# Kernel tuning notes

Hardware: AMD Instinct MI355X
Metric: run time of the kernel (lower is better)

Reference implementation:

```python
import jax, jax.numpy as jnp
import numpy as np

H = 256
EPS = 1e-5
RBF_GAMMA = 10.0
RBF_CENTERS = jnp.asarray(np.arange(0.0, np.pi, 0.1), dtype=jnp.float32)  # 32 centers


def layer_norm(x, g, b):
    m = x.mean(-1, keepdims=True)
    v = ((x - m) ** 2).mean(-1, keepdims=True)
    return (x - m) * jax.lax.rsqrt(v + EPS) * g + b


def gin(src, dst, n_nodes, node_feat, edge_feat, w1, b1, w2, b2):
    # message = h_src + h_edge ; sum-aggregate at dst ; 2-layer MLP
    msg = node_feat[src] + edge_feat                                  # [E, H]
    agg = jax.ops.segment_sum(msg, dst, num_segments=n_nodes)        # [N, H]
    return jax.nn.relu(agg @ w1 + b1) @ w2 + b2


def graph_normal(gid, n_graphs, x):
    # divide each node feature by sqrt(#nodes in its graph)
    cnt = jax.ops.segment_sum(jnp.ones((x.shape[0],), x.dtype), gid, num_segments=n_graphs)
    return x * jax.lax.rsqrt(jnp.maximum(cnt, 1.0))[gid][:, None]


def geognn_block(src, dst, gid, n_graphs, node_hidden, edge_feat, w1, b1, w2, b2, ln_g, ln_b):
    out = gin(src, dst, node_hidden.shape[0], node_hidden, edge_feat, w1, b1, w2, b2)
    out = layer_norm(out, ln_g, ln_b)
    out = graph_normal(gid, n_graphs, out)
    # activation=False, dropout is identity in eval mode
    return out + node_hidden


def setup_inputs() -> dict:
    key = jax.random.key(0)
    ks = jax.random.split(key, 24)
    N, E, A, G = 65536, 131072, 262144, 2048
    nC = RBF_CENTERS.shape[0]
    s = 1.0 / np.sqrt(H)
    inp = {
        "node_hidden": jax.random.normal(ks[0], (N, H), jnp.float32),
        "edge_hidden": jax.random.normal(ks[1], (E, H), jnp.float32),
        "bond_angle": jax.random.uniform(ks[2], (A,), jnp.float32) * np.float32(np.pi),
        "ab_src": jax.random.randint(ks[3], (N * 2,), 0, N).astype(jnp.int64)[:E],
        "ab_dst": jax.random.randint(ks[4], (E,), 0, N).astype(jnp.int64),
        "ba_src": jax.random.randint(ks[5], (A,), 0, E).astype(jnp.int64),
        "ba_dst": jax.random.randint(ks[6], (A,), 0, E).astype(jnp.int64),
        "node_gid": jnp.sort(jax.random.randint(ks[7], (N,), 0, G)).astype(jnp.int64),
        "bond_gid": jnp.sort(jax.random.randint(ks[8], (E,), 0, G)).astype(jnp.int64),
        "num_graphs": G,
        # bond-angle RBF linear
        "rbf_w": jax.random.normal(ks[9], (nC, H), jnp.float32) / np.sqrt(nC),
        "rbf_b": jnp.zeros((H,), jnp.float32),
        # bond_angle_gnn (GIN MLP + LayerNorm)
        "ba_w1": jax.random.normal(ks[10], (H, 2 * H), jnp.float32) * s,
        "ba_b1": jnp.zeros((2 * H,), jnp.float32),
        "ba_w2": jax.random.normal(ks[11], (2 * H, H), jnp.float32) * s,
        "ba_b2": jnp.zeros((H,), jnp.float32),
        "ba_ln_g": jnp.ones((H,), jnp.float32),
        "ba_ln_b": jnp.zeros((H,), jnp.float32),
        # atom_bond_gnn
        "ab_w1": jax.random.normal(ks[12], (H, 2 * H), jnp.float32) * s,
        "ab_b1": jnp.zeros((2 * H,), jnp.float32),
        "ab_w2": jax.random.normal(ks[13], (2 * H, H), jnp.float32) * s,
        "ab_b2": jnp.zeros((H,), jnp.float32),
        "ab_ln_g": jnp.ones((H,), jnp.float32),
        "ab_ln_b": jnp.zeros((H,), jnp.float32),
    }
    return inp


def reference(node_hidden, edge_hidden, bond_angle, ab_src, ab_dst, ba_src, ba_dst,
              node_gid, bond_gid, num_graphs, rbf_w, rbf_b,
              ba_w1, ba_b1, ba_w2, ba_b2, ba_ln_g, ba_ln_b,
              ab_w1, ab_b1, ab_w2, ab_b2, ab_ln_g, ab_ln_b):
    # RBF encode bond angles -> angle edge features [A, H]
    rbf = jnp.exp(-RBF_GAMMA * (bond_angle[:, None] - RBF_CENTERS[None, :]) ** 2)
    angle_hidden = rbf @ rbf_w + rbf_b
    # bond-angle GNN updates bond features (nodes of bond_angle graph)
    edge_out = geognn_block(ba_src, ba_dst, bond_gid, num_graphs,
                            edge_hidden, angle_hidden,
                            ba_w1, ba_b1, ba_w2, ba_b2, ba_ln_g, ba_ln_b)
    # atom-bond GNN updates atom features using updated bond features as edge feats
    node_out = geognn_block(ab_src, ab_dst, node_gid, num_graphs,
                            node_hidden, edge_out,
                            ab_w1, ab_b1, ab_w2, ab_b2, ab_ln_g, ab_ln_b)
    # average pooling over atoms per graph
    cnt = jax.ops.segment_sum(jnp.ones((node_out.shape[0],), node_out.dtype), node_gid,
                              num_segments=num_graphs)
    graph_repr = jax.ops.segment_sum(node_out, node_gid, num_segments=num_graphs) / jnp.maximum(cnt, 1.0)[:, None]
    return node_out, edge_out, graph_repr
```

## Files before the change

### kernel.cpp

```cpp
#include <hip/hip_runtime.h>

#define HDIM 256
#define LNEPS 1e-5f

typedef float f32x4 __attribute__((ext_vector_type(4)));
typedef short bf16x8 __attribute__((ext_vector_type(8)));

static __device__ __forceinline__ unsigned short f2b(float f) {
  union { float f; unsigned u; } v; v.f = f;
  return (unsigned short)((v.u + 0x7fffu + ((v.u >> 16) & 1u)) >> 16);
}
static __device__ __forceinline__ unsigned pk2(float lo, float hi) {
  return (unsigned)f2b(lo) | ((unsigned)f2b(hi) << 16);
}

__global__ void pack1_kernel(const float* __restrict__ in, unsigned short* __restrict__ out) {
  int o = blockIdx.x * 256 + threadIdx.x;
  int ke = o & 7, n1l = (o >> 3) & 127, lg = (o >> 10) & 3, sl = o >> 12;
  int h = sl >> 3, kk = sl & 7;
  int k = kk * 32 + lg * 8 + ke, n1 = h * 128 + n1l;
  out[o] = f2b(in[k * 512 + n1]);
}

__global__ void pack2_kernel(const float* __restrict__ in, unsigned short* __restrict__ out) {
  int o = blockIdx.x * 256 + threadIdx.x;
  int ke = o & 7, n2l = (o >> 3) & 127, lg = (o >> 10) & 3, sl = o >> 12;
  int h = sl >> 3, r = sl & 7, h2 = r >> 2, kk2 = r & 3;
  int k2 = h * 128 + kk2 * 32 + lg * 8 + ke, n2 = h2 * 128 + n2l;
  out[o] = f2b(in[k2 * 256 + n2]);
}

__global__ void count_kernel(const int* __restrict__ node_gid, const int* __restrict__ bond_gid,
                             int* cnt_node, int* cnt_bond, int N, int E) {
  int i = blockIdx.x * 256 + threadIdx.x;
  if (i < N) atomicAdd(&cnt_node[node_gid[i]], 1);
  if (i < E) atomicAdd(&cnt_bond[bond_gid[i]], 1);
}

__global__ void factor_kernel(const int* __restrict__ cnt_node, const int* __restrict__ cnt_bond,
                              float* fac_node, float* fac_bond, float* recip_node, int G) {
  int g = blockIdx.x * 256 + threadIdx.x;
  if (g >= G) return;
  float cn = fmaxf((float)cnt_node[g], 1.f);
  float cb = fmaxf((float)cnt_bond[g], 1.f);
  fac_node[g] = rsqrtf(cn);
  fac_bond[g] = rsqrtf(cb);
  recip_node[g] = 1.f / cn;
}

__global__ void deg_kernel(const int* __restrict__ dst, int* __restrict__ deg, int n) {
  int i = blockIdx.x * 256 + threadIdx.x;
  if (i < n) atomicAdd(&deg[dst[i]], 1);
}

__global__ void scan1_kernel(const int* __restrict__ deg, int* __restrict__ excl,
                             int* __restrict__ bsum, int n) {
  int t = threadIdx.x;
  int i = blockIdx.x * 256 + t;
  int v = (i < n) ? deg[i] : 0;
  int lane = t & 63, w = t >> 6;
  int s = v;
#pragma unroll
  for (int d = 1; d < 64; d <<= 1) {
    int u = __shfl_up(s, d);
    if (lane >= d) s += u;
  }
  __shared__ int wsum[4];
  if (lane == 63) wsum[w] = s;
  __syncthreads();
  int base = 0;
  for (int ww = 0; ww < w; ++ww) base += wsum[ww];
  if (i < n) excl[i] = base + s - v;
  if (t == 255) bsum[blockIdx.x] = base + s;
}

__global__ void scan2_kernel(int* __restrict__ bsum, int nb) {
  int t = threadIdx.x;
  int v = (t < nb) ? bsum[t] : 0;
  int lane = t & 63, w = t >> 6;
  int s = v;
#pragma unroll
  for (int d = 1; d < 64; d <<= 1) {
    int u = __shfl_up(s, d);
    if (lane >= d) s += u;
  }
  __shared__ int wsum[16];
  if (lane == 63) wsum[w] = s;
  __syncthreads();
  int base = 0;
  for (int ww = 0; ww < w; ++ww) base += wsum[ww];
  if (t < nb) bsum[t] = base + s - v;
}

__global__ void scan3_kernel(int* __restrict__ excl, const int* __restrict__ bsum, int n) {
  int i = blockIdx.x * 256 + threadIdx.x;
  if (i < n) excl[i] += bsum[blockIdx.x];
}

__global__ void fill_kernel(const int* __restrict__ dst, const int* __restrict__ off,
                            int* __restrict__ cursor, int* __restrict__ csr, int n) {
  int i = blockIdx.x * 256 + threadIdx.x;
  if (i >= n) return;
  int d = dst[i];
  int p = atomicAdd(&cursor[d], 1);
  csr[off[d] + p] = i;
}

__global__ __launch_bounds__(256) void angle_gather_kernel(
    const float* __restrict__ bond_angle, const int* __restrict__ ba_src,
    const float* __restrict__ edge_hidden,
    const int* __restrict__ off, const int* __restrict__ deg, const int* __restrict__ csr,
    const float* __restrict__ rbf_w, const float* __restrict__ rbf_b,
    float* __restrict__ agg_e, int E) {
  __shared__ float rbfw_s[32 * 256];
  int t = threadIdx.x;
  int w = t >> 6, lane = t & 63;
#pragma unroll
  for (int i = 0; i < 8; ++i)
    *(f32x4*)&rbfw_s[(t + i * 256) * 4] = *(const f32x4*)&rbf_w[(t + i * 256) * 4];
  __syncthreads();
  int c4 = lane * 4;
  f32x4 bv = *(const f32x4*)&rbf_b[c4];
  float cc = 0.1f * (float)(lane & 31);
  for (int rr = 0; rr < 2; ++rr) {
    int d = blockIdx.x * 8 + w * 2 + rr;
    if (d >= E) break;
    int start = off[d], cnt = deg[d];
    f32x4 acc = (f32x4)0.f;
    float rbfs = 0.f;
    for (int base = 0; base < cnt; base += 64) {
      int n = cnt - base; if (n > 64) n = 64;
      float av = 0.f;
      int s = 0;
      if (lane < n) {
        int a = csr[start + base + lane];
        av = bond_angle[a];
        s = ba_src[a];
      }
#pragma unroll 4
      for (int i = 0; i < n; ++i) {
        float avi = __shfl(av, i);
        int si = __shfl(s, i);
        if (lane < 32) {
          float dd = avi - cc;
          rbfs += __expf(-10.f * dd * dd);
        }
        acc += *(const f32x4*)&edge_hidden[(size_t)si * HDIM + c4];
      }
    }
#pragma unroll 8
    for (int k = 0; k < 32; ++k) {
      float rv = __shfl(rbfs, k);
      f32x4 wv = *(const f32x4*)&rbfw_s[k * 256 + c4];
      acc[0] += rv * wv[0]; acc[1] += rv * wv[1];
      acc[2] += rv * wv[2]; acc[3] += rv * wv[3];
    }
    float fc = (float)cnt;
    acc[0] += fc * bv[0]; acc[1] += fc * bv[1];
    acc[2] += fc * bv[2]; acc[3] += fc * bv[3];
    *(f32x4*)&agg_e[(size_t)d * HDIM + c4] = acc;
  }
}

__global__ __launch_bounds__(256) void node_gather_kernel(
    const float* __restrict__ node_hidden, const float* __restrict__ edge_out,
    const int* __restrict__ ab_src,
    const int* __restrict__ off, const int* __restrict__ deg, const int* __restrict__ csr,
    float* __restrict__ agg_n, int N) {
  int w = threadIdx.x >> 6, lane = threadIdx.x & 63;
  int d = blockIdx.x * 4 + w;
  if (d >= N) return;
  int c4 = lane * 4;
  int start = off[d], cnt = deg[d];
  f32x4 acc = (f32x4)0.f;
  for (int base = 0; base < cnt; base += 64) {
    int n = cnt - base; if (n > 64) n = 64;
    int e = 0, s = 0;
    if (lane < n) {
      e = csr[start + base + lane];
      s = ab_src[e];
    }
#pragma unroll 4
    for (int i = 0; i < n; ++i) {
      int ei = __shfl(e, i);
      int si = __shfl(s, i);
      f32x4 a = *(const f32x4*)&edge_out[(size_t)ei * HDIM + c4];
      f32x4 b = *(const f32x4*)&node_hidden[(size_t)si * HDIM + c4];
      acc += a;
      acc += b;
    }
  }
  *(f32x4*)&agg_n[(size_t)d * HDIM + c4] = acc;
}

template <int POOL>
__global__ __launch_bounds__(256, 4) void mlp_kernel(
    const float* agg_in, float* out_rows,
    const float* __restrict__ residual, const int* __restrict__ gid,
    const float* __restrict__ gfactor,
    const unsigned short* __restrict__ w1p, const float* __restrict__ b1,
    const unsigned short* __restrict__ w2p, const float* __restrict__ b2,
    const float* __restrict__ ln_g, const float* __restrict__ ln_b,
    float* pool_out, int M) {
  __shared__ __align__(16) char smem[40960];
  char* Xb = smem;
  char* Hb = smem + 16384;
  char* Wb = smem + 24576;
  float* Outs = (float*)smem;
  float* fstat = (float*)(smem + 40448);
  float* gfs = (float*)(smem + 40704);
  int* gid_s = (int*)(smem + 40832);

  int t = threadIdx.x;
  int row0 = blockIdx.x * 32;
  int w = t >> 6, lane = t & 63;
  int l15 = lane & 15, lg = lane >> 4;

  auto slab_ptr = [&](int ss) -> const uint4* {
    int hh = ss >> 4, r = ss & 15;
    const unsigned short* p = (r < 8) ? (w1p + (size_t)(hh * 8 + r) * 4096)
                                      : (w2p + (size_t)(hh * 8 + (r - 8)) * 4096);
    return (const uint4*)p;
  };

  uint4 rA0, rA1, rB0, rB1;

  {
    const uint4* g0 = slab_ptr(0);
    uint4 s0a = g0[t], s0b = g0[t + 256];
    const uint4* g1 = slab_ptr(1);
    rA0 = g1[t]; rA1 = g1[t + 256];
    int row = t >> 3;
    int c0 = (t & 7) * 32;
    int gr = row0 + row; if (gr >= M) gr = M - 1;
    const float* src = agg_in + (size_t)gr * HDIM + c0;
#pragma unroll
    for (int i = 0; i < 4; ++i) {
      f32x4 a = *(const f32x4*)(src + i * 8);
      f32x4 b = *(const f32x4*)(src + i * 8 + 4);
      int byte = (row * 512 + (c0 + i * 8) * 2) ^ ((row & 7) << 4);
      *(uint4*)(Xb + byte) =
          make_uint4(pk2(a[0], a[1]), pk2(a[2], a[3]), pk2(b[0], b[1]), pk2(b[2], b[3]));
    }
    *(uint4*)(Wb + t * 16) = s0a;
    *(uint4*)(Wb + (t + 256) * 16) = s0b;
  }
  __syncthreads();

  f32x4 acc2[2][4];
#pragma unroll
  for (int mt = 0; mt < 2; ++mt)
#pragma unroll
    for (int nf = 0; nf < 4; ++nf) acc2[mt][nf] = (f32x4)0.f;

  int s = 0;
  for (int h = 0; h < 4; ++h) {
    f32x4 acc1[2][2];
#pragma unroll
    for (int tt = 0; tt < 2; ++tt)
#pragma unroll
      for (int mt = 0; mt < 2; ++mt) acc1[tt][mt] = (f32x4)0.f;

    for (int kk = 0; kk < 8; ++kk) {
      if (s + 2 < 64) { const uint4* g = slab_ptr(s + 2); rB0 = g[t]; rB1 = g[t + 256]; }
      const char* buf = Wb + (s & 1) * 8192;
      bf16x8 xfr[2], afr[2];
#pragma unroll
      for (int mt = 0; mt < 2; ++mt) {
        int m = mt * 16 + l15;
        int byte = (m * 512 + kk * 64 + lg * 16) ^ ((m & 7) << 4);
        xfr[mt] = *(const bf16x8*)(Xb + byte);
      }
#pragma unroll
      for (int tt = 0; tt < 2; ++tt)
        afr[tt] = *(const bf16x8*)(buf + lg * 2048 + (w * 32 + tt * 16 + l15) * 16);
#pragma unroll
      for (int tt = 0; tt < 2; ++tt)
#pragma unroll
        for (int mt = 0; mt < 2; ++mt)
          acc1[tt][mt] = __builtin_amdgcn_mfma_f32_16x16x32_bf16(afr[tt], xfr[mt], acc1[tt][mt], 0, 0, 0);

      if (kk == 7) {
#pragma unroll
        for (int tt = 0; tt < 2; ++tt) {
          f32x4 b1v = *(const f32x4*)&b1[h * 128 + w * 32 + tt * 16 + lg * 4];
#pragma unroll
          for (int mt = 0; mt < 2; ++mt) {
            f32x4 v = acc1[tt][mt] + b1v;
            v[0] = fmaxf(v[0], 0.f); v[1] = fmaxf(v[1], 0.f);
            v[2] = fmaxf(v[2], 0.f); v[3] = fmaxf(v[3], 0.f);
            int m = mt * 16 + l15;
            int n1l = w * 32 + tt * 16 + lg * 4;
            int byte = (m * 256 + n1l * 2) ^ ((m & 7) << 4);
            *(uint2*)(Hb + byte) = make_uint2(pk2(v[0], v[1]), pk2(v[2], v[3]));
          }
        }
      }
      if (s + 1 < 64) {
        char* nb = Wb + ((s + 1) & 1) * 8192;
        *(uint4*)(nb + t * 16) = rA0;
        *(uint4*)(nb + (t + 256) * 16) = rA1;
      }
      __syncthreads();
      rA0 = rB0; rA1 = rB1;
      ++s;
    }

#pragma unroll
    for (int h2 = 0; h2 < 2; ++h2) {
#pragma unroll
      for (int kk2 = 0; kk2 < 4; ++kk2) {
        if (s + 2 < 64) { const uint4* g = slab_ptr(s + 2); rB0 = g[t]; rB1 = g[t + 256]; }
        const char* buf = Wb + (s & 1) * 8192;
        bf16x8 hfr[2], wfr[2];
#pragma unroll
        for (int mt = 0; mt < 2; ++mt) {
          int m = mt * 16 + l15;
          int byte = (m * 256 + kk2 * 64 + lg * 16) ^ ((m & 7) << 4);
          hfr[mt] = *(const bf16x8*)(Hb + byte);
        }
#pragma unroll
        for (int nf = 0; nf < 2; ++nf)
          wfr[nf] = *(const bf16x8*)(buf + lg * 2048 + (w * 32 + nf * 16 + l15) * 16);
#pragma unroll
        for (int mt = 0; mt < 2; ++mt)
#pragma unroll
          for (int nf = 0; nf < 2; ++nf)
            acc2[mt][h2 * 2 + nf] =
                __builtin_amdgcn_mfma_f32_16x16x32_bf16(hfr[mt], wfr[nf], acc2[mt][h2 * 2 + nf], 0, 0, 0);
        if (s + 1 < 64) {
          char* nb = Wb + ((s + 1) & 1) * 8192;
          *(uint4*)(nb + t * 16) = rA0;
          *(uint4*)(nb + (t + 256) * 16) = rA1;
        }
        __syncthreads();
        rA0 = rB0; rA1 = rB1;
        ++s;
      }
    }
  }

#pragma unroll
  for (int nf = 0; nf < 4; ++nf) {
    int col = (nf >> 1) * 128 + w * 32 + (nf & 1) * 16 + l15;
    float b2v = b2[col];
#pragma unroll
    for (int mt = 0; mt < 2; ++mt)
#pragma unroll
      for (int jr = 0; jr < 4; ++jr)
        Outs[(mt * 16 + lg * 4 + jr) * 256 + col] = acc2[mt][nf][jr] + b2v;
  }
  if (t < 32) {
    int r = row0 + t;
    int g = (r < M) ? gid[r] : 0;
    gid_s[t] = g;
    gfs[t] = gfactor[g];
  }
  __syncthreads();

  {
    int row = t >> 3, sub = t & 7;
    float ssum = 0.f, ss = 0.f;
#pragma unroll
    for (int i = 0; i < 8; ++i) {
      f32x4 v = *(const f32x4*)&Outs[row * 256 + sub * 32 + i * 4];
      ssum += v[0] + v[1] + v[2] + v[3];
      ss += v[0] * v[0] + v[1] * v[1] + v[2] * v[2] + v[3] * v[3];
    }
    ssum += __shfl_xor(ssum, 1); ss += __shfl_xor(ss, 1);
    ssum += __shfl_xor(ssum, 2); ss += __shfl_xor(ss, 2);
    ssum += __shfl_xor(ssum, 4); ss += __shfl_xor(ss, 4);
    if (sub == 0) {
      float mean = ssum * (1.f / 256.f);
      float var = ss * (1.f / 256.f) - mean * mean;
      fstat[row * 2] = mean;
      fstat[row * 2 + 1] = rsqrtf(var + LNEPS);
    }
  }
  __syncthreads();

  {
    float g_t = ln_g[t], bb_t = ln_b[t];
    float psum = 0.f;
    int curg = -1;
#pragma unroll 4
    for (int p = 0; p < 32; ++p) {
      int gr = row0 + p;
      if (gr < M) {
        float v = Outs[p * 256 + t];
        v = (v - fstat[p * 2]) * fstat[p * 2 + 1] * g_t + bb_t;
        v *= gfs[p];
        v += residual[(size_t)gr * HDIM + t];
        out_rows[(size_t)gr * HDIM + t] = v;
        if (POOL) {
          int g = gid_s[p];
          if (g != curg) {
            if (curg >= 0) atomicAdd(&pool_out[(size_t)curg * HDIM + t], psum);
            psum = 0.f;
            curg = g;
          }
          psum += v;
        }
      }
    }
    if (POOL && curg >= 0) atomicAdd(&pool_out[(size_t)curg * HDIM + t], psum);
  }
}

__global__ void pooldiv_kernel(float* out_graph, const float* __restrict__ recip_node) {
  int g = blockIdx.x, t = threadIdx.x;
  out_graph[(size_t)g * HDIM + t] *= recip_node[g];
}

extern "C" void kernel_launch(void* const* d_in, const int* in_sizes, int n_in,
                              void* d_out, int out_size, void* d_ws, size_t ws_size,
                              hipStream_t stream) {
  const float* node_hidden = (const float*)d_in[0];
  const float* edge_hidden = (const float*)d_in[1];
  const float* bond_angle = (const float*)d_in[2];
  const int* ab_src = (const int*)d_in[3];
  const int* ab_dst = (const int*)d_in[4];
  const int* ba_src = (const int*)d_in[5];
  const int* ba_dst = (const int*)d_in[6];
  const int* node_gid = (const int*)d_in[7];
  const int* bond_gid = (const int*)d_in[8];
  const float* rbf_w = (const float*)d_in[10];
  const float* rbf_b = (const float*)d_in[11];
  const float* ba_w1 = (const float*)d_in[12];
  const float* ba_b1 = (const float*)d_in[13];
  const float* ba_w2 = (const float*)d_in[14];
  const float* ba_b2 = (const float*)d_in[15];
  const float* ba_ln_g = (const float*)d_in[16];
  const float* ba_ln_b = (const float*)d_in[17];
  const float* ab_w1 = (const float*)d_in[18];
  const float* ab_b1 = (const float*)d_in[19];
  const float* ab_w2 = (const float*)d_in[20];
  const float* ab_b2 = (const float*)d_in[21];
  const float* ab_ln_g = (const float*)d_in[22];
  const float* ab_ln_b = (const float*)d_in[23];

  int N = in_sizes[0] / HDIM;
  int E = in_sizes[1] / HDIM;
  int A = in_sizes[2];
  int G = out_size / HDIM - N - E;

  float* out_node = (float*)d_out;
  float* out_edge = out_node + (size_t)N * HDIM;
  float* out_graph = out_edge + (size_t)E * HDIM;

  char* ws = (char*)d_ws;
  int* cnt_node = (int*)ws;
  int* cnt_bond = cnt_node + G;
  int* deg_e = cnt_bond + G;
  int* cur_e = deg_e + E;
  int* deg_n = cur_e + E;
  int* cur_n = deg_n + N;
  size_t zero_bytes = (size_t)(2 * G + 2 * E + 2 * N) * 4;
  float* fac_node = (float*)(cur_n + N);
  float* fac_bond = fac_node + G;
  float* recip_node = fac_bond + G;
  int* off_e = (int*)(recip_node + G);
  int* csr_e = off_e + E;
  int* off_n = csr_e + A;
  int* csr_n = off_n + N;
  int* bsum = csr_n + E;
  size_t off = ((size_t)((char*)(bsum + 1024) - ws) + 255) & ~(size_t)255;
  unsigned short* w1p_ba = (unsigned short*)(ws + off); off += (size_t)512 * 256 * 2;
  unsigned short* w2p_ba = (unsigned short*)(ws + off); off += (size_t)256 * 512 * 2;
  unsigned short* w1p_ab = (unsigned short*)(ws + off); off += (size_t)512 * 256 * 2;
  unsigned short* w2p_ab = (unsigned short*)(ws + off); off += (size_t)256 * 512 * 2;

  hipMemsetAsync(d_ws, 0, zero_bytes, stream);
  hipMemsetAsync(out_graph, 0, (size_t)G * HDIM * 4, stream);

  pack1_kernel<<<512, 256, 0, stream>>>(ba_w1, w1p_ba);
  pack2_kernel<<<512, 256, 0, stream>>>(ba_w2, w2p_ba);
  pack1_kernel<<<512, 256, 0, stream>>>(ab_w1, w1p_ab);
  pack2_kernel<<<512, 256, 0, stream>>>(ab_w2, w2p_ab);

  count_kernel<<<(E + 255) / 256, 256, 0, stream>>>(node_gid, bond_gid, cnt_node, cnt_bond, N, E);
  factor_kernel<<<(G + 255) / 256, 256, 0, stream>>>(cnt_node, cnt_bond, fac_node, fac_bond,
                                                     recip_node, G);

  deg_kernel<<<(A + 255) / 256, 256, 0, stream>>>(ba_dst, deg_e, A);
  int nbE = (E + 255) / 256;
  scan1_kernel<<<nbE, 256, 0, stream>>>(deg_e, off_e, bsum, E);
  scan2_kernel<<<1, 1024, 0, stream>>>(bsum, nbE);
  scan3_kernel<<<nbE, 256, 0, stream>>>(off_e, bsum, E);
  fill_kernel<<<(A + 255) / 256, 256, 0, stream>>>(ba_dst, off_e, cur_e, csr_e, A);

  angle_gather_kernel<<<(E + 7) / 8, 256, 0, stream>>>(bond_angle, ba_src, edge_hidden,
                                                       off_e, deg_e, csr_e, rbf_w, rbf_b,
                                                       out_edge, E);
  mlp_kernel<0><<<(E + 31) / 32, 256, 0, stream>>>(out_edge, out_edge, edge_hidden, bond_gid,
                                                   fac_bond, w1p_ba, ba_b1, w2p_ba, ba_b2,
                                                   ba_ln_g, ba_ln_b, nullptr, E);

  deg_kernel<<<(E + 255) / 256, 256, 0, stream>>>(ab_dst, deg_n, E);
  int nbN = (N + 255) / 256;
  scan1_kernel<<<nbN, 256, 0, stream>>>(deg_n, off_n, bsum, N);
  scan2_kernel<<<1, 1024, 0, stream>>>(bsum, nbN);
  scan3_kernel<<<nbN, 256, 0, stream>>>(off_n, bsum, N);
  fill_kernel<<<(E + 255) / 256, 256, 0, stream>>>(ab_dst, off_n, cur_n, csr_n, E);

  node_gather_kernel<<<(N + 3) / 4, 256, 0, stream>>>(node_hidden, out_edge, ab_src,
                                                      off_n, deg_n, csr_n, out_node, N);
  mlp_kernel<1><<<(N + 31) / 32, 256, 0, stream>>>(out_node, out_node, node_hidden, node_gid,
                                                   fac_node, w1p_ab, ab_b1, w2p_ab, ab_b2,
                                                   ab_ln_g, ab_ln_b, out_graph, N);

  pooldiv_kernel<<<G, 256, 0, stream>>>(out_graph, recip_node);
}
```

Measured before the change: 610.7 us.

## Load MLP weight fragments directly from global into registers, drop LDS weight staging

The weight packing is reordered so that each wave's lanes can read their MFMA B-fragments straight from global memory. The MLP kernel drops the LDS double-buffered weight slabs and the per-slab block barrier, and prefetches fragments two steps ahead in registers. LayerNorm statistics are now computed from the accumulators with shuffles and a small cross-wave partial-sum array instead of re-reading the staged output. This cuts LDS use and most __syncthreads, at the cost of every wave fetching its own weight fragments from cache and using more registers.

```diff
diff --git a/kernel.cpp b/kernel.cpp
--- a/kernel.cpp
+++ b/kernel.cpp
@@ -16,17 +16,21 @@
 
 __global__ void pack1_kernel(const float* __restrict__ in, unsigned short* __restrict__ out) {
   int o = blockIdx.x * 256 + threadIdx.x;
-  int ke = o & 7, n1l = (o >> 3) & 127, lg = (o >> 10) & 3, sl = o >> 12;
+  int ke = o & 7, lane = (o >> 3) & 63, ttw = (o >> 9) & 7, sl = o >> 12;
   int h = sl >> 3, kk = sl & 7;
-  int k = kk * 32 + lg * 8 + ke, n1 = h * 128 + n1l;
+  int l15 = lane & 15, lg = lane >> 4;
+  int n1 = h * 128 + (ttw >> 1) * 32 + (ttw & 1) * 16 + l15;
+  int k = kk * 32 + lg * 8 + ke;
   out[o] = f2b(in[k * 512 + n1]);
 }
 
 __global__ void pack2_kernel(const float* __restrict__ in, unsigned short* __restrict__ out) {
   int o = blockIdx.x * 256 + threadIdx.x;
-  int ke = o & 7, n2l = (o >> 3) & 127, lg = (o >> 10) & 3, sl = o >> 12;
-  int h = sl >> 3, r = sl & 7, h2 = r >> 2, kk2 = r & 3;
-  int k2 = h * 128 + kk2 * 32 + lg * 8 + ke, n2 = h2 * 128 + n2l;
+  int ke = o & 7, lane = (o >> 3) & 63, ttw = (o >> 9) & 7, sl = o >> 12;
+  int h = sl >> 3, h2 = (sl >> 2) & 1, kk2 = sl & 3;
+  int l15 = lane & 15, lg = lane >> 4;
+  int n2 = h2 * 128 + (ttw >> 1) * 32 + (ttw & 1) * 16 + l15;
+  int k2 = h * 128 + kk2 * 32 + lg * 8 + ke;
   out[o] = f2b(in[k2 * 256 + n2]);
 }
 
@@ -202,34 +206,31 @@
     const unsigned short* __restrict__ w2p, const float* __restrict__ b2,
     const float* __restrict__ ln_g, const float* __restrict__ ln_b,
     float* pool_out, int M) {
-  __shared__ __align__(16) char smem[40960];
+  __shared__ __align__(16) char smem[34304];
   char* Xb = smem;
   char* Hb = smem + 16384;
-  char* Wb = smem + 24576;
   float* Outs = (float*)smem;
-  float* fstat = (float*)(smem + 40448);
-  float* gfs = (float*)(smem + 40704);
-  int* gid_s = (int*)(smem + 40832);
+  float* psA = (float*)(smem + 32768);
+  float* psB = (float*)(smem + 33280);
+  float* fstat = (float*)(smem + 33792);
+  float* gfs = (float*)(smem + 34048);
+  int* gid_s = (int*)(smem + 34176);
 
   int t = threadIdx.x;
   int row0 = blockIdx.x * 32;
   int w = t >> 6, lane = t & 63;
   int l15 = lane & 15, lg = lane >> 4;
 
-  auto slab_ptr = [&](int ss) -> const uint4* {
-    int hh = ss >> 4, r = ss & 15;
-    const unsigned short* p = (r < 8) ? (w1p + (size_t)(hh * 8 + r) * 4096)
-                                      : (w2p + (size_t)(hh * 8 + (r - 8)) * 4096);
-    return (const uint4*)p;
-  };
-
-  uint4 rA0, rA1, rB0, rB1;
+#define W1F(hh, kk, tt) \
+  (*(const bf16x8*)(w1p + ((size_t)(((hh) * 8 + (kk)) * 8 + w * 2 + (tt)) * 64 + lane) * 8))
+#define W2F(hh, q, nf) \
+  (*(const bf16x8*)(w2p + ((size_t)(((hh) * 8 + (q)) * 8 + w * 2 + (nf)) * 64 + lane) * 8))
+
+  bf16x8 wq[2][2], wq2[2][2];
+  wq[0][0] = W1F(0, 0, 0); wq[0][1] = W1F(0, 0, 1);
+  wq[1][0] = W1F(0, 1, 0); wq[1][1] = W1F(0, 1, 1);
 
   {
-    const uint4* g0 = slab_ptr(0);
-    uint4 s0a = g0[t], s0b = g0[t + 256];
-    const uint4* g1 = slab_ptr(1);
-    rA0 = g1[t]; rA1 = g1[t + 256];
     int row = t >> 3;
     int c0 = (t & 7) * 32;
     int gr = row0 + row; if (gr >= M) gr = M - 1;
@@ -242,8 +243,6 @@
       *(uint4*)(Xb + byte) =
           make_uint4(pk2(a[0], a[1]), pk2(a[2], a[3]), pk2(b[0], b[1]), pk2(b[2], b[3]));
     }
-    *(uint4*)(Wb + t * 16) = s0a;
-    *(uint4*)(Wb + (t + 256) * 16) = s0b;
   }
   __syncthreads();
 
@@ -253,7 +252,6 @@
 #pragma unroll
     for (int nf = 0; nf < 4; ++nf) acc2[mt][nf] = (f32x4)0.f;
 
-  int s = 0;
   for (int h = 0; h < 4; ++h) {
     f32x4 acc1[2][2];
 #pragma unroll
@@ -261,121 +259,129 @@
 #pragma unroll
       for (int mt = 0; mt < 2; ++mt) acc1[tt][mt] = (f32x4)0.f;
 
+#pragma unroll
     for (int kk = 0; kk < 8; ++kk) {
-      if (s + 2 < 64) { const uint4* g = slab_ptr(s + 2); rB0 = g[t]; rB1 = g[t + 256]; }
-      const char* buf = Wb + (s & 1) * 8192;
-      bf16x8 xfr[2], afr[2];
+      bf16x8 a0 = wq[kk & 1][0], a1 = wq[kk & 1][1];
+      bf16x8 xfr0, xfr1;
+      {
+        int byte = (l15 * 512 + kk * 64 + lg * 16) ^ ((l15 & 7) << 4);
+        xfr0 = *(const bf16x8*)(Xb + byte);
+      }
+      {
+        int m = 16 + l15;
+        int byte = (m * 512 + kk * 64 + lg * 16) ^ ((m & 7) << 4);
+        xfr1 = *(const bf16x8*)(Xb + byte);
+      }
+      if (kk < 6) {
+        wq[kk & 1][0] = W1F(h, kk + 2, 0);
+        wq[kk & 1][1] = W1F(h, kk + 2, 1);
+      } else {
+        wq2[kk - 6][0] = W2F(h, kk - 6, 0);
+        wq2[kk - 6][1] = W2F(h, kk - 6, 1);
+      }
+      acc1[0][0] = __builtin_amdgcn_mfma_f32_16x16x32_bf16(a0, xfr0, acc1[0][0], 0, 0, 0);
+      acc1[0][1] = __builtin_amdgcn_mfma_f32_16x16x32_bf16(a0, xfr1, acc1[0][1], 0, 0, 0);
+      acc1[1][0] = __builtin_amdgcn_mfma_f32_16x16x32_bf16(a1, xfr0, acc1[1][0], 0, 0, 0);
+      acc1[1][1] = __builtin_amdgcn_mfma_f32_16x16x32_bf16(a1, xfr1, acc1[1][1], 0, 0, 0);
+    }
+
+#pragma unroll
+    for (int tt = 0; tt < 2; ++tt) {
+      f32x4 b1v = *(const f32x4*)&b1[h * 128 + w * 32 + tt * 16 + lg * 4];
 #pragma unroll
       for (int mt = 0; mt < 2; ++mt) {
+        f32x4 v = acc1[tt][mt] + b1v;
+        v[0] = fmaxf(v[0], 0.f); v[1] = fmaxf(v[1], 0.f);
+        v[2] = fmaxf(v[2], 0.f); v[3] = fmaxf(v[3], 0.f);
         int m = mt * 16 + l15;
-        int byte = (m * 512 + kk * 64 + lg * 16) ^ ((m & 7) << 4);
-        xfr[mt] = *(const bf16x8*)(Xb + byte);
-      }
-#pragma unroll
-      for (int tt = 0; tt < 2; ++tt)
-        afr[tt] = *(const bf16x8*)(buf + lg * 2048 + (w * 32 + tt * 16 + l15) * 16);
-#pragma unroll
-      for (int tt = 0; tt < 2; ++tt)
-#pragma unroll
-        for (int mt = 0; mt < 2; ++mt)
-          acc1[tt][mt] = __builtin_amdgcn_mfma_f32_16x16x32_bf16(afr[tt], xfr[mt], acc1[tt][mt], 0, 0, 0);
-
-      if (kk == 7) {
-#pragma unroll
-        for (int tt = 0; tt < 2; ++tt) {
-          f32x4 b1v = *(const f32x4*)&b1[h * 128 + w * 32 + tt * 16 + lg * 4];
-#pragma unroll
-          for (int mt = 0; mt < 2; ++mt) {
-            f32x4 v = acc1[tt][mt] + b1v;
-            v[0] = fmaxf(v[0], 0.f); v[1] = fmaxf(v[1], 0.f);
-            v[2] = fmaxf(v[2], 0.f); v[3] = fmaxf(v[3], 0.f);
-            int m = mt * 16 + l15;
-            int n1l = w * 32 + tt * 16 + lg * 4;
-            int byte = (m * 256 + n1l * 2) ^ ((m & 7) << 4);
-            *(uint2*)(Hb + byte) = make_uint2(pk2(v[0], v[1]), pk2(v[2], v[3]));
-          }
+        int n1l = w * 32 + tt * 16 + lg * 4;
+        int byte = (m * 256 + n1l * 2) ^ ((m & 7) << 4);
+        *(uint2*)(Hb + byte) = make_uint2(pk2(v[0], v[1]), pk2(v[2], v[3]));
+      }
+    }
+    __syncthreads();
+
+#pragma unroll
+    for (int q = 0; q < 8; ++q) {
+      bf16x8 b0 = wq2[q & 1][0], b1f = wq2[q & 1][1];
+      int kk2 = q & 3, h2 = q >> 2;
+      bf16x8 hfr0, hfr1;
+      {
+        int byte = (l15 * 256 + kk2 * 64 + lg * 16) ^ ((l15 & 7) << 4);
+        hfr0 = *(const bf16x8*)(Hb + byte);
+      }
+      {
+        int m = 16 + l15;
+        int byte = (m * 256 + kk2 * 64 + lg * 16) ^ ((m & 7) << 4);
+        hfr1 = *(const bf16x8*)(Hb + byte);
+      }
+      if (q < 6) {
+        wq2[q & 1][0] = W2F(h, q + 2, 0);
+        wq2[q & 1][1] = W2F(h, q + 2, 1);
+      } else if (h < 3) {
+        wq[q - 6][0] = W1F(h + 1, q - 6, 0);
+        wq[q - 6][1] = W1F(h + 1, q - 6, 1);
+      }
+      acc2[0][h2 * 2 + 0] = __builtin_amdgcn_mfma_f32_16x16x32_bf16(hfr0, b0, acc2[0][h2 * 2 + 0], 0, 0, 0);
+      acc2[0][h2 * 2 + 1] = __builtin_amdgcn_mfma_f32_16x16x32_bf16(hfr0, b1f, acc2[0][h2 * 2 + 1], 0, 0, 0);
+      acc2[1][h2 * 2 + 0] = __builtin_amdgcn_mfma_f32_16x16x32_bf16(hfr1, b0, acc2[1][h2 * 2 + 0], 0, 0, 0);
+      acc2[1][h2 * 2 + 1] = __builtin_amdgcn_mfma_f32_16x16x32_bf16(hfr1, b1f, acc2[1][h2 * 2 + 1], 0, 0, 0);
+    }
+    __syncthreads();
+  }
+#undef W1F
+#undef W2F
+
+  {
+    float rs[2][4], rss[2][4];
+#pragma unroll
+    for (int mt = 0; mt < 2; ++mt)
+#pragma unroll
+      for (int jr = 0; jr < 4; ++jr) { rs[mt][jr] = 0.f; rss[mt][jr] = 0.f; }
+#pragma unroll
+    for (int nfi = 0; nfi < 4; ++nfi) {
+      int col = (nfi >> 1) * 128 + w * 32 + (nfi & 1) * 16 + l15;
+      float b2v = b2[col];
+#pragma unroll
+      for (int mt = 0; mt < 2; ++mt)
+#pragma unroll
+        for (int jr = 0; jr < 4; ++jr) {
+          float v = acc2[mt][nfi][jr] + b2v;
+          Outs[(mt * 16 + lg * 4 + jr) * 256 + col] = v;
+          rs[mt][jr] += v;
+          rss[mt][jr] += v * v;
         }
-      }
-      if (s + 1 < 64) {
-        char* nb = Wb + ((s + 1) & 1) * 8192;
-        *(uint4*)(nb + t * 16) = rA0;
-        *(uint4*)(nb + (t + 256) * 16) = rA1;
-      }
-      __syncthreads();
-      rA0 = rB0; rA1 = rB1;
-      ++s;
-    }
-
-#pragma unroll
-    for (int h2 = 0; h2 < 2; ++h2) {
-#pragma unroll
-      for (int kk2 = 0; kk2 < 4; ++kk2) {
-        if (s + 2 < 64) { const uint4* g = slab_ptr(s + 2); rB0 = g[t]; rB1 = g[t + 256]; }
-        const char* buf = Wb + (s & 1) * 8192;
-        bf16x8 hfr[2], wfr[2];
-#pragma unroll
-        for (int mt = 0; mt < 2; ++mt) {
-          int m = mt * 16 + l15;
-          int byte = (m * 256 + kk2 * 64 + lg * 16) ^ ((m & 7) << 4);
-          hfr[mt] = *(const bf16x8*)(Hb + byte);
+    }
+#pragma unroll
+    for (int mt = 0; mt < 2; ++mt)
+#pragma unroll
+      for (int jr = 0; jr < 4; ++jr) {
+        float s = rs[mt][jr], ss = rss[mt][jr];
+        s += __shfl_xor(s, 1); ss += __shfl_xor(ss, 1);
+        s += __shfl_xor(s, 2); ss += __shfl_xor(ss, 2);
+        s += __shfl_xor(s, 4); ss += __shfl_xor(ss, 4);
+        s += __shfl_xor(s, 8); ss += __shfl_xor(ss, 8);
+        if (l15 == 0) {
+          int r = mt * 16 + lg * 4 + jr;
+          psA[r * 4 + w] = s;
+          psB[r * 4 + w] = ss;
         }
-#pragma unroll
-        for (int nf = 0; nf < 2; ++nf)
-          wfr[nf] = *(const bf16x8*)(buf + lg * 2048 + (w * 32 + nf * 16 + l15) * 16);
-#pragma unroll
-        for (int mt = 0; mt < 2; ++mt)
-#pragma unroll
-          for (int nf = 0; nf < 2; ++nf)
-            acc2[mt][h2 * 2 + nf] =
-                __builtin_amdgcn_mfma_f32_16x16x32_bf16(hfr[mt], wfr[nf], acc2[mt][h2 * 2 + nf], 0, 0, 0);
-        if (s + 1 < 64) {
-          char* nb = Wb + ((s + 1) & 1) * 8192;
-          *(uint4*)(nb + t * 16) = rA0;
-          *(uint4*)(nb + (t + 256) * 16) = rA1;
-        }
-        __syncthreads();
-        rA0 = rB0; rA1 = rB1;
-        ++s;
-      }
-    }
-  }
-
-#pragma unroll
-  for (int nf = 0; nf < 4; ++nf) {
-    int col = (nf >> 1) * 128 + w * 32 + (nf & 1) * 16 + l15;
-    float b2v = b2[col];
-#pragma unroll
-    for (int mt = 0; mt < 2; ++mt)
-#pragma unroll
-      for (int jr = 0; jr < 4; ++jr)
-        Outs[(mt * 16 + lg * 4 + jr) * 256 + col] = acc2[mt][nf][jr] + b2v;
-  }
+      }
+    if (t < 32) {
+      int r = row0 + t;
+      int g = (r < M) ? gid[r] : 0;
+      gid_s[t] = g;
+      gfs[t] = gfactor[g];
+    }
+  }
+  __syncthreads();
   if (t < 32) {
-    int r = row0 + t;
-    int g = (r < M) ? gid[r] : 0;
-    gid_s[t] = g;
-    gfs[t] = gfactor[g];
-  }
-  __syncthreads();
-
-  {
-    int row = t >> 3, sub = t & 7;
-    float ssum = 0.f, ss = 0.f;
-#pragma unroll
-    for (int i = 0; i < 8; ++i) {
-      f32x4 v = *(const f32x4*)&Outs[row * 256 + sub * 32 + i * 4];
-      ssum += v[0] + v[1] + v[2] + v[3];
-      ss += v[0] * v[0] + v[1] * v[1] + v[2] * v[2] + v[3] * v[3];
-    }
-    ssum += __shfl_xor(ssum, 1); ss += __shfl_xor(ss, 1);
-    ssum += __shfl_xor(ssum, 2); ss += __shfl_xor(ss, 2);
-    ssum += __shfl_xor(ssum, 4); ss += __shfl_xor(ss, 4);
-    if (sub == 0) {
-      float mean = ssum * (1.f / 256.f);
-      float var = ss * (1.f / 256.f) - mean * mean;
-      fstat[row * 2] = mean;
-      fstat[row * 2 + 1] = rsqrtf(var + LNEPS);
-    }
+    float s = psA[t * 4] + psA[t * 4 + 1] + psA[t * 4 + 2] + psA[t * 4 + 3];
+    float ss = psB[t * 4] + psB[t * 4 + 1] + psB[t * 4 + 2] + psB[t * 4 + 3];
+    float mean = s * (1.f / 256.f);
+    float var = ss * (1.f / 256.f) - mean * mean;
+    fstat[t * 2] = mean;
+    fstat[t * 2 + 1] = rsqrtf(var + LNEPS);
   }
   __syncthreads();
 
```

New measurement: 819.0 us. +34.1%, slower.

## Merge preprocessing launches and compute LayerNorm stats from MFMA accumulators

Applied to the files above, without the earlier changes.

Replaces the many small setup kernels (weight packing, counts, degree, scan, fill) with a few combined kernels that cover both graphs at once, cutting the number of kernel launches roughly in half. The MLP epilogue now takes LayerNorm row sums and sums of squares directly from the accumulator registers through shuffles, instead of re-reading the whole output tile from shared memory. It also XOR-swizzles the shared-memory output tile to reduce bank conflicts. The scan buffer is split at offset 512 per graph, which assumes each graph needs at most 512 partial-sum blocks.

```diff
diff --git a/kernel.cpp b/kernel.cpp
--- a/kernel.cpp
+++ b/kernel.cpp
@@ -14,49 +14,51 @@
   return (unsigned)f2b(lo) | ((unsigned)f2b(hi) << 16);
 }
 
-__global__ void pack1_kernel(const float* __restrict__ in, unsigned short* __restrict__ out) {
-  int o = blockIdx.x * 256 + threadIdx.x;
-  int ke = o & 7, n1l = (o >> 3) & 127, lg = (o >> 10) & 3, sl = o >> 12;
-  int h = sl >> 3, kk = sl & 7;
-  int k = kk * 32 + lg * 8 + ke, n1 = h * 128 + n1l;
-  out[o] = f2b(in[k * 512 + n1]);
-}
-
-__global__ void pack2_kernel(const float* __restrict__ in, unsigned short* __restrict__ out) {
-  int o = blockIdx.x * 256 + threadIdx.x;
-  int ke = o & 7, n2l = (o >> 3) & 127, lg = (o >> 10) & 3, sl = o >> 12;
-  int h = sl >> 3, r = sl & 7, h2 = r >> 2, kk2 = r & 3;
-  int k2 = h * 128 + kk2 * 32 + lg * 8 + ke, n2 = h2 * 128 + n2l;
-  out[o] = f2b(in[k2 * 256 + n2]);
-}
-
-__global__ void count_kernel(const int* __restrict__ node_gid, const int* __restrict__ bond_gid,
-                             int* cnt_node, int* cnt_bond, int N, int E) {
+__global__ void pack_all_kernel(const float* __restrict__ w1a, const float* __restrict__ w2a,
+                                const float* __restrict__ w1b, const float* __restrict__ w2b,
+                                unsigned short* __restrict__ o1a, unsigned short* __restrict__ o2a,
+                                unsigned short* __restrict__ o1b, unsigned short* __restrict__ o2b) {
+  int sel = blockIdx.x >> 9;
+  int o = (blockIdx.x & 511) * 256 + threadIdx.x;
+  if (sel == 0 || sel == 2) {
+    const float* in = (sel == 0) ? w1a : w1b;
+    unsigned short* out = (sel == 0) ? o1a : o1b;
+    int ke = o & 7, n1l = (o >> 3) & 127, lg = (o >> 10) & 3, sl = o >> 12;
+    int h = sl >> 3, kk = sl & 7;
+    int k = kk * 32 + lg * 8 + ke, n1 = h * 128 + n1l;
+    out[o] = f2b(in[k * 512 + n1]);
+  } else {
+    const float* in = (sel == 1) ? w2a : w2b;
+    unsigned short* out = (sel == 1) ? o2a : o2b;
+    int ke = o & 7, n2l = (o >> 3) & 127, lg = (o >> 10) & 3, sl = o >> 12;
+    int h = sl >> 3, r = sl & 7, h2 = r >> 2, kk2 = r & 3;
+    int k2 = h * 128 + kk2 * 32 + lg * 8 + ke, n2 = h2 * 128 + n2l;
+    out[o] = f2b(in[k2 * 256 + n2]);
+  }
+}
+
+__global__ void prep_kernel(const int* __restrict__ node_gid, const int* __restrict__ bond_gid,
+                            const int* __restrict__ ab_dst, const int* __restrict__ ba_dst,
+                            int* cnt_node, int* cnt_bond, int* deg_n, int* deg_e,
+                            int N, int E, int A) {
   int i = blockIdx.x * 256 + threadIdx.x;
   if (i < N) atomicAdd(&cnt_node[node_gid[i]], 1);
-  if (i < E) atomicAdd(&cnt_bond[bond_gid[i]], 1);
-}
-
-__global__ void factor_kernel(const int* __restrict__ cnt_node, const int* __restrict__ cnt_bond,
-                              float* fac_node, float* fac_bond, float* recip_node, int G) {
-  int g = blockIdx.x * 256 + threadIdx.x;
-  if (g >= G) return;
-  float cn = fmaxf((float)cnt_node[g], 1.f);
-  float cb = fmaxf((float)cnt_bond[g], 1.f);
-  fac_node[g] = rsqrtf(cn);
-  fac_bond[g] = rsqrtf(cb);
-  recip_node[g] = 1.f / cn;
-}
-
-__global__ void deg_kernel(const int* __restrict__ dst, int* __restrict__ deg, int n) {
-  int i = blockIdx.x * 256 + threadIdx.x;
-  if (i < n) atomicAdd(&deg[dst[i]], 1);
-}
-
-__global__ void scan1_kernel(const int* __restrict__ deg, int* __restrict__ excl,
-                             int* __restrict__ bsum, int n) {
+  if (i < E) {
+    atomicAdd(&cnt_bond[bond_gid[i]], 1);
+    atomicAdd(&deg_n[ab_dst[i]], 1);
+  }
+  if (i < A) atomicAdd(&deg_e[ba_dst[i]], 1);
+}
+
+__global__ void scan1_both_kernel(const int* __restrict__ degE, const int* __restrict__ degN,
+                                  int* __restrict__ offE, int* __restrict__ offN,
+                                  int* __restrict__ bsum, int E, int N, int nbE) {
+  int b = blockIdx.x;
+  const int* deg; int* excl; int* bs; int n; int bb;
+  if (b < nbE) { deg = degE; excl = offE; bs = bsum; n = E; bb = b; }
+  else { deg = degN; excl = offN; bs = bsum + 512; n = N; bb = b - nbE; }
   int t = threadIdx.x;
-  int i = blockIdx.x * 256 + t;
+  int i = bb * 256 + t;
   int v = (i < n) ? deg[i] : 0;
   int lane = t & 63, w = t >> 6;
   int s = v;
@@ -71,12 +73,14 @@
   int base = 0;
   for (int ww = 0; ww < w; ++ww) base += wsum[ww];
   if (i < n) excl[i] = base + s - v;
-  if (t == 255) bsum[blockIdx.x] = base + s;
-}
-
-__global__ void scan2_kernel(int* __restrict__ bsum, int nb) {
+  if (t == 255) bs[bb] = base + s;
+}
+
+__global__ void scan2_both_kernel(int* __restrict__ bsum, int nbE, int nbN) {
+  int* bs = bsum + blockIdx.x * 512;
+  int nb = (blockIdx.x == 0) ? nbE : nbN;
   int t = threadIdx.x;
-  int v = (t < nb) ? bsum[t] : 0;
+  int v = (t < nb) ? bs[t] : 0;
   int lane = t & 63, w = t >> 6;
   int s = v;
 #pragma unroll
@@ -89,21 +93,55 @@
   __syncthreads();
   int base = 0;
   for (int ww = 0; ww < w; ++ww) base += wsum[ww];
-  if (t < nb) bsum[t] = base + s - v;
-}
-
-__global__ void scan3_kernel(int* __restrict__ excl, const int* __restrict__ bsum, int n) {
-  int i = blockIdx.x * 256 + threadIdx.x;
-  if (i < n) excl[i] += bsum[blockIdx.x];
-}
-
-__global__ void fill_kernel(const int* __restrict__ dst, const int* __restrict__ off,
-                            int* __restrict__ cursor, int* __restrict__ csr, int n) {
-  int i = blockIdx.x * 256 + threadIdx.x;
-  if (i >= n) return;
-  int d = dst[i];
-  int p = atomicAdd(&cursor[d], 1);
-  csr[off[d] + p] = i;
+  if (t < nb) bs[t] = base + s - v;
+}
+
+__global__ void scan3f_kernel(int* __restrict__ offE, int* __restrict__ offN,
+                              const int* __restrict__ bsum,
+                              const int* __restrict__ cnt_node, const int* __restrict__ cnt_bond,
+                              float* fac_node, float* fac_bond, float* recip_node,
+                              int E, int N, int G, int nbE, int nbN) {
+  int b = blockIdx.x;
+  if (b < nbE) {
+    int i = b * 256 + threadIdx.x;
+    if (i < E) offE[i] += bsum[b];
+  } else if (b < nbE + nbN) {
+    int bb = b - nbE;
+    int i = bb * 256 + threadIdx.x;
+    if (i < N) offN[i] += bsum[512 + bb];
+  } else {
+    int g = (b - nbE - nbN) * 256 + threadIdx.x;
+    if (g < G) {
+      float cn = fmaxf((float)cnt_node[g], 1.f);
+      float cb = fmaxf((float)cnt_bond[g], 1.f);
+      fac_node[g] = rsqrtf(cn);
+      fac_bond[g] = rsqrtf(cb);
+      recip_node[g] = 1.f / cn;
+    }
+  }
+}
+
+__global__ void fill_both_kernel(const int* __restrict__ ba_dst, const int* __restrict__ ab_dst,
+                                 const int* __restrict__ offE, const int* __restrict__ offN,
+                                 int* __restrict__ curE, int* __restrict__ curN,
+                                 int* __restrict__ csrE, int* __restrict__ csrN,
+                                 int A, int E, int nbA) {
+  int b = blockIdx.x;
+  if (b < nbA) {
+    int i = b * 256 + threadIdx.x;
+    if (i < A) {
+      int d = ba_dst[i];
+      int p = atomicAdd(&curE[d], 1);
+      csrE[offE[d] + p] = i;
+    }
+  } else {
+    int i = (b - nbA) * 256 + threadIdx.x;
+    if (i < E) {
+      int d = ab_dst[i];
+      int p = atomicAdd(&curN[d], 1);
+      csrN[offN[d] + p] = i;
+    }
+  }
 }
 
 __global__ __launch_bounds__(256) void angle_gather_kernel(
@@ -206,10 +244,12 @@
   char* Xb = smem;
   char* Hb = smem + 16384;
   char* Wb = smem + 24576;
-  float* Outs = (float*)smem;
-  float* fstat = (float*)(smem + 40448);
-  float* gfs = (float*)(smem + 40704);
-  int* gid_s = (int*)(smem + 40832);
+  char* OutsB = smem;
+  float* psA = (float*)(smem + 32768);
+  float* psB = (float*)(smem + 33280);
+  float* fstat = (float*)(smem + 33792);
+  float* gfs = (float*)(smem + 34048);
+  int* gid_s = (int*)(smem + 34176);
 
   int t = threadIdx.x;
   int row0 = blockIdx.x * 32;
@@ -340,42 +380,57 @@
     }
   }
 
-#pragma unroll
-  for (int nf = 0; nf < 4; ++nf) {
-    int col = (nf >> 1) * 128 + w * 32 + (nf & 1) * 16 + l15;
-    float b2v = b2[col];
+  {
+    float rs[2][4], rss[2][4];
 #pragma unroll
     for (int mt = 0; mt < 2; ++mt)
 #pragma unroll
-      for (int jr = 0; jr < 4; ++jr)
-        Outs[(mt * 16 + lg * 4 + jr) * 256 + col] = acc2[mt][nf][jr] + b2v;
-  }
+      for (int jr = 0; jr < 4; ++jr) { rs[mt][jr] = 0.f; rss[mt][jr] = 0.f; }
+#pragma unroll
+    for (int nfi = 0; nfi < 4; ++nfi) {
+      int col = (nfi >> 1) * 128 + w * 32 + (nfi & 1) * 16 + l15;
+      float b2v = b2[col];
+#pragma unroll
+      for (int mt = 0; mt < 2; ++mt)
+#pragma unroll
+        for (int jr = 0; jr < 4; ++jr) {
+          float v = acc2[mt][nfi][jr] + b2v;
+          int row = mt * 16 + lg * 4 + jr;
+          *(float*)(OutsB + (((row * 256 + col) * 4) ^ ((row & 7) << 4))) = v;
+          rs[mt][jr] += v;
+          rss[mt][jr] += v * v;
+        }
+    }
+#pragma unroll
+    for (int mt = 0; mt < 2; ++mt)
+#pragma unroll
+      for (int jr = 0; jr < 4; ++jr) {
+        float sv = rs[mt][jr], ssv = rss[mt][jr];
+        sv += __shfl_xor(sv, 1); ssv += __shfl_xor(ssv, 1);
+        sv += __shfl_xor(sv, 2); ssv += __shfl_xor(ssv, 2);
+        sv += __shfl_xor(sv, 4); ssv += __shfl_xor(ssv, 4);
+        sv += __shfl_xor(sv, 8); ssv += __shfl_xor(ssv, 8);
+        if (l15 == 0) {
+          int r = mt * 16 + lg * 4 + jr;
+          psA[r * 4 + w] = sv;
+          psB[r * 4 + w] = ssv;
+        }
+      }
+    if (t < 32) {
+      int r = row0 + t;
+      int g = (r < M) ? gid[r] : 0;
+      gid_s[t] = g;
+      gfs[t] = gfactor[g];
+    }
+  }
+  __syncthreads();
   if (t < 32) {
-    int r = row0 + t;
-    int g = (r < M) ? gid[r] : 0;
-    gid_s[t] = g;
-    gfs[t] = gfactor[g];
-  }
-  __syncthreads();
-
-  {
-    int row = t >> 3, sub = t & 7;
-    float ssum = 0.f, ss = 0.f;
-#pragma unroll
-    for (int i = 0; i < 8; ++i) {
-      f32x4 v = *(const f32x4*)&Outs[row * 256 + sub * 32 + i * 4];
-      ssum += v[0] + v[1] + v[2] + v[3];
-      ss += v[0] * v[0] + v[1] * v[1] + v[2] * v[2] + v[3] * v[3];
-    }
-    ssum += __shfl_xor(ssum, 1); ss += __shfl_xor(ss, 1);
-    ssum += __shfl_xor(ssum, 2); ss += __shfl_xor(ss, 2);
-    ssum += __shfl_xor(ssum, 4); ss += __shfl_xor(ss, 4);
-    if (sub == 0) {
-      float mean = ssum * (1.f / 256.f);
-      float var = ss * (1.f / 256.f) - mean * mean;
-      fstat[row * 2] = mean;
-      fstat[row * 2 + 1] = rsqrtf(var + LNEPS);
-    }
+    float sv = psA[t * 4] + psA[t * 4 + 1] + psA[t * 4 + 2] + psA[t * 4 + 3];
+    float ssv = psB[t * 4] + psB[t * 4 + 1] + psB[t * 4 + 2] + psB[t * 4 + 3];
+    float mean = sv * (1.f / 256.f);
+    float var = ssv * (1.f / 256.f) - mean * mean;
+    fstat[t * 2] = mean;
+    fstat[t * 2 + 1] = rsqrtf(var + LNEPS);
   }
   __syncthreads();
 
@@ -387,7 +442,7 @@
     for (int p = 0; p < 32; ++p) {
       int gr = row0 + p;
       if (gr < M) {
-        float v = Outs[p * 256 + t];
+        float v = *(const float*)(OutsB + (((p * 256 + t) * 4) ^ ((p & 7) << 4)));
         v = (v - fstat[p * 2]) * fstat[p * 2 + 1] * g_t + bb_t;
         v *= gfs[p];
         v += residual[(size_t)gr * HDIM + t];
@@ -473,21 +528,23 @@
   hipMemsetAsync(d_ws, 0, zero_bytes, stream);
   hipMemsetAsync(out_graph, 0, (size_t)G * HDIM * 4, stream);
 
-  pack1_kernel<<<512, 256, 0, stream>>>(ba_w1, w1p_ba);
-  pack2_kernel<<<512, 256, 0, stream>>>(ba_w2, w2p_ba);
-  pack1_kernel<<<512, 256, 0, stream>>>(ab_w1, w1p_ab);
-  pack2_kernel<<<512, 256, 0, stream>>>(ab_w2, w2p_ab);
-
-  count_kernel<<<(E + 255) / 256, 256, 0, stream>>>(node_gid, bond_gid, cnt_node, cnt_bond, N, E);
-  factor_kernel<<<(G + 255) / 256, 256, 0, stream>>>(cnt_node, cnt_bond, fac_node, fac_bond,
-                                                     recip_node, G);
-
-  deg_kernel<<<(A + 255) / 256, 256, 0, stream>>>(ba_dst, deg_e, A);
+  pack_all_kernel<<<2048, 256, 0, stream>>>(ba_w1, ba_w2, ab_w1, ab_w2,
+                                            w1p_ba, w2p_ba, w1p_ab, w2p_ab);
+
+  prep_kernel<<<(A + 255) / 256, 256, 0, stream>>>(node_gid, bond_gid, ab_dst, ba_dst,
+                                                   cnt_node, cnt_bond, deg_n, deg_e, N, E, A);
+
   int nbE = (E + 255) / 256;
-  scan1_kernel<<<nbE, 256, 0, stream>>>(deg_e, off_e, bsum, E);
-  scan2_kernel<<<1, 1024, 0, stream>>>(bsum, nbE);
-  scan3_kernel<<<nbE, 256, 0, stream>>>(off_e, bsum, E);
-  fill_kernel<<<(A + 255) / 256, 256, 0, stream>>>(ba_dst, off_e, cur_e, csr_e, A);
+  int nbN = (N + 255) / 256;
+  int nbA = (A + 255) / 256;
+  int nbG = (G + 255) / 256;
+  scan1_both_kernel<<<nbE + nbN, 256, 0, stream>>>(deg_e, deg_n, off_e, off_n, bsum, E, N, nbE);
+  scan2_both_kernel<<<2, 1024, 0, stream>>>(bsum, nbE, nbN);
+  scan3f_kernel<<<nbE + nbN + nbG, 256, 0, stream>>>(off_e, off_n, bsum, cnt_node, cnt_bond,
+                                                     fac_node, fac_bond, recip_node,
+                                                     E, N, G, nbE, nbN);
+  fill_both_kernel<<<nbA + nbE, 256, 0, stream>>>(ba_dst, ab_dst, off_e, off_n,
+                                                  cur_e, cur_n, csr_e, csr_n, A, E, nbA);
 
   angle_gather_kernel<<<(E + 7) / 8, 256, 0, stream>>>(bond_angle, ba_src, edge_hidden,
                                                        off_e, deg_e, csr_e, rbf_w, rbf_b,
@@ -496,13 +553,6 @@
                                                    fac_bond, w1p_ba, ba_b1, w2p_ba, ba_b2,
                                                    ba_ln_g, ba_ln_b, nullptr, E);
 
-  deg_kernel<<<(E + 255) / 256, 256, 0, stream>>>(ab_dst, deg_n, E);
-  int nbN = (N + 255) / 256;
-  scan1_kernel<<<nbN, 256, 0, stream>>>(deg_n, off_n, bsum, N);
-  scan2_kernel<<<1, 1024, 0, stream>>>(bsum, nbN);
-  scan3_kernel<<<nbN, 256, 0, stream>>>(off_n, bsum, N);
-  fill_kernel<<<(E + 255) / 256, 256, 0, stream>>>(ab_dst, off_n, cur_n, csr_n, E);
-
   node_gather_kernel<<<(N + 3) / 4, 256, 0, stream>>>(node_hidden, out_edge, ab_src,
                                                       off_n, deg_n, csr_n, out_node, N);
   mlp_kernel<1><<<(N + 31) / 32, 256, 0, stream>>>(out_node, out_node, node_hidden, node_gid,
```

New measurement: 593.8 us. 2.8% less time.
